# Kernel tuning notes

Hardware: AMD Instinct MI355X
Metric: run time of the kernel (lower is better)

Reference implementation:

```python
import jax, jax.numpy as jnp
import numpy as np

SOS = 1  # vocab.word2idx[SYM_SOS]


def _lstm_cell(x, h, c, Wih, Whh, b):
    # PyTorch LSTMCell gate order: i, f, g, o
    g = x @ Wih.T + h @ Whh.T + b
    i, f, gg, o = jnp.split(g, 4, axis=-1)
    c2 = jax.nn.sigmoid(f) * c + jax.nn.sigmoid(i) * jnp.tanh(gg)
    h2 = jax.nn.sigmoid(o) * jnp.tanh(c2)
    return h2, c2


def _attention(q, m, Wq, Wm, b, v):
    # additive attention: q [B,Dq], m [B,N,Dm] -> context [B,Dm]
    e = jnp.tanh((q @ Wq)[:, None, :] + m @ Wm + b)      # [B,N,H]
    score = jnp.einsum('bnh,h->bn', e, v)                # [B,N]
    a = jax.nn.softmax(score, axis=-1)
    return jnp.einsum('bn,bnd->bd', a, m)


def setup_inputs() -> dict:
    key = jax.random.key(0)
    ks = iter(jax.random.split(key, 32))
    B, T, V = 128, 20, 20000
    DI, DW, H = 512, 512, 1024
    s = 0.02
    d = {}
    d['img_feats'] = jax.random.normal(next(ks), (B, 36, DI), jnp.float32)
    d['ppl_feats'] = jax.random.normal(next(ks), (B, 100, DI), jnp.float32)
    d['answer_hint'] = jax.random.normal(next(ks), (B, DW), jnp.float32)
    d['question'] = jax.random.randint(next(ks), (B, T), 0, V)
    d['emb'] = jax.random.normal(next(ks), (V, DW), jnp.float32) * s
    d['pool_Wq'] = jax.random.normal(next(ks), (DW, DW), jnp.float32) * s
    d['pool_Wm'] = jax.random.normal(next(ks), (DI, DW), jnp.float32) * s
    d['pool_b'] = jnp.zeros((DW,), jnp.float32)
    d['pool_v'] = jax.random.normal(next(ks), (DW,), jnp.float32) * s
    d['img_Wq'] = jax.random.normal(next(ks), (H, H), jnp.float32) * s
    d['img_Wm'] = jax.random.normal(next(ks), (DI, H), jnp.float32) * s
    d['img_b'] = jnp.zeros((H,), jnp.float32)
    d['img_v'] = jax.random.normal(next(ks), (H,), jnp.float32) * s
    d['ppl_Wq'] = jax.random.normal(next(ks), (H, H), jnp.float32) * s
    d['ppl_Wm'] = jax.random.normal(next(ks), (DI, H), jnp.float32) * s
    d['ppl_b'] = jnp.zeros((H,), jnp.float32)
    d['ppl_v'] = jax.random.normal(next(ks), (H,), jnp.float32) * s
    d['vis_Wih'] = jax.random.normal(next(ks), (4 * H, DI + DW), jnp.float32) * s
    d['vis_Whh'] = jax.random.normal(next(ks), (4 * H, H), jnp.float32) * s
    d['vis_b'] = jnp.zeros((4 * H,), jnp.float32)
    d['lang_Wih'] = jax.random.normal(next(ks), (4 * H, H + DI), jnp.float32) * s
    d['lang_Whh'] = jax.random.normal(next(ks), (4 * H, H), jnp.float32) * s
    d['lang_b'] = jnp.zeros((4 * H,), jnp.float32)
    d['proj_W'] = jax.random.normal(next(ks), (H, V), jnp.float32) * s
    d['proj_b'] = jnp.zeros((V,), jnp.float32)
    return d


def reference(img_feats, ppl_feats, answer_hint, question, emb,
              pool_Wq, pool_Wm, pool_b, pool_v,
              img_Wq, img_Wm, img_b, img_v,
              ppl_Wq, ppl_Wm, ppl_b, ppl_v,
              vis_Wih, vis_Whh, vis_b,
              lang_Wih, lang_Whh, lang_b,
              proj_W, proj_b):
    B, T = question.shape
    H = vis_Whh.shape[1]
    # pooled image feature from answer hint (computed once)
    img_pool = _attention(answer_hint, img_feats, pool_Wq, pool_Wm, pool_b, pool_v)
    # teacher forcing inputs: SOS then question[:, :-1]
    tokens_in = jnp.concatenate(
        [jnp.full((B, 1), SOS, question.dtype), question[:, :-1]], axis=1)

    def step(carry, tok):
        h_vis, c_vis, h_lang, c_lang = carry
        dec_emb = jax.nn.relu(emb[tok])                          # [B,DW]
        x_vis = jnp.concatenate([img_pool, dec_emb], axis=-1)
        h_vis, c_vis = _lstm_cell(x_vis, h_vis, c_vis, vis_Wih, vis_Whh, vis_b)
        image_attn = _attention(h_vis, img_feats, img_Wq, img_Wm, img_b, img_v)
        ppl_attn = _attention(h_vis, ppl_feats, ppl_Wq, ppl_Wm, ppl_b, ppl_v)
        x_lang = jnp.concatenate([image_attn + ppl_attn, h_vis], axis=-1)
        h_lang, c_lang = _lstm_cell(x_lang, h_lang, c_lang, lang_Wih, lang_Whh, lang_b)
        logp = jax.nn.log_softmax(h_lang @ proj_W + proj_b, axis=-1)
        return (h_vis, c_vis, h_lang, c_lang), (logp, jnp.argmax(logp, axis=-1))

    z = jnp.zeros((B, H), img_feats.dtype)
    _, (logps, toks) = jax.lax.scan(step, (z, z, z, z), tokens_in.T)
    return jnp.transpose(logps, (1, 0, 2)), toks.T


if __name__ == '__main__':
    out = reference(**setup_inputs())
    print(out[0].shape, out[1].shape)
```

## Files before the change

### kernel.cpp

```cpp
#include <hip/hip_runtime.h>
#include <cstddef>
#include <cstdint>

using u16 = unsigned short;
typedef float    f32x4 __attribute__((ext_vector_type(4)));
typedef _Float16 f16x8 __attribute__((ext_vector_type(8)));
typedef u16      us8   __attribute__((ext_vector_type(8)));

constexpr int B  = 128;
constexpr int T  = 20;
constexpr int V  = 20000;
constexpr int DW = 512;
constexpr int H  = 1024;
constexpr int G4 = 4096;
constexpr int NI = 36;
constexpr int NP = 100;
constexpr int SOS = 1;

__device__ __forceinline__ float sigf(float x) { return 1.0f / (1.0f + expf(-x)); }
__device__ __forceinline__ u16 f16bits(_Float16 h) { u16 u; __builtin_memcpy(&u, &h, 2); return u; }
__device__ __forceinline__ float h2f(u16 u) { _Float16 h; __builtin_memcpy(&h, &u, 2); return (float)h; }

template<bool WSIDE>
__device__ __forceinline__ void split1(float x, u16& b0, u16& b1, u16& b2) {
    _Float16 h  = (_Float16)x;
    float    hf = (float)h;
    _Float16 lo = (_Float16)((x - hf) * 64.0f);
    _Float16 hs = (_Float16)(hf * (1.0f / 64.0f));
    b0 = f16bits(h);
    if constexpr (WSIDE) { b1 = f16bits(hs); b2 = f16bits(lo); }
    else                 { b1 = f16bits(lo); b2 = f16bits(hs); }
}

template<int BM, int BN, bool HAS_ADD, bool HAS_BIAS, int NSW = 0, bool OUTF16 = false>
__global__ __launch_bounds__(256)
void gemm3(const u16* __restrict__ A, const u16* __restrict__ Bt,
           const float* __restrict__ Add, const float* __restrict__ bias,
           void* __restrict__ Cv, int N, int K3)
{
    __shared__ __align__(16) u16 As[BM * 64];
    __shared__ __align__(16) u16 Bs[BN * 64];
    constexpr int FR = BM / 32, FC = BN / 32, PA = BM / 32, PB = BN / 32;
    const int tid  = threadIdx.x;
    int bx = blockIdx.x, by = blockIdx.y;
    if constexpr (NSW > 0) {
        const int nt = (int)gridDim.x, mt = (int)gridDim.y;
        const int lin = by * nt + bx;
        const int sc0 = (lin / (NSW * mt)) * NSW;
        const int w   = (NSW < nt - sc0) ? NSW : (nt - sc0);
        const int r   = lin - sc0 * mt;
        bx = sc0 + r % w;
        by = r / w;
    }
    const int bm   = by * BM, bn = bx * BN;
    const int lane = tid & 63, wid = tid >> 6;
    const int wm   = (wid >> 1) * (BM / 2), wn = (wid & 1) * (BN / 2);
    const int srow = tid >> 3;
    const int scol = (tid & 7) * 8;

    f32x4 acc[FR][FC] = {};
    us8 ra[PA], rb[PB];

    auto ldg = [&](int k0) {
#pragma unroll
        for (int p = 0; p < PA; ++p)
            ra[p] = *(const us8*)(A + (size_t)(bm + p * 32 + srow) * K3 + k0 + scol);
#pragma unroll
        for (int p = 0; p < PB; ++p) {
            int n = bn + p * 32 + srow; if (n > N - 1) n = N - 1;
            rb[p] = *(const us8*)(Bt + (size_t)n * K3 + k0 + scol);
        }
    };
    ldg(0);

    for (int k0 = 0; k0 < K3; k0 += 64) {
        __syncthreads();
#pragma unroll
        for (int p = 0; p < PA; ++p) {
            const int row = p * 32 + srow;
            *(us8*)((char*)As + row * 128 + ((scol * 2) ^ ((row & 7) << 4))) = ra[p];
        }
#pragma unroll
        for (int p = 0; p < PB; ++p) {
            const int row = p * 32 + srow;
            *(us8*)((char*)Bs + row * 128 + ((scol * 2) ^ ((row & 7) << 4))) = rb[p];
        }
        __syncthreads();
        if (k0 + 64 < K3) ldg(k0 + 64);
#pragma unroll
        for (int ks = 0; ks < 2; ++ks) {
            f16x8 af[FR], bf[FC];
#pragma unroll
            for (int m = 0; m < FR; ++m) {
                const int row = wm + m * 16 + (lane & 15);
                const int cb  = (ks * 64 + ((lane >> 4) << 4)) ^ ((row & 7) << 4);
                af[m] = *(const f16x8*)((const char*)As + row * 128 + cb);
            }
#pragma unroll
            for (int n = 0; n < FC; ++n) {
                const int row = wn + n * 16 + (lane & 15);
                const int cb  = (ks * 64 + ((lane >> 4) << 4)) ^ ((row & 7) << 4);
                bf[n] = *(const f16x8*)((const char*)Bs + row * 128 + cb);
            }
#pragma unroll
            for (int m = 0; m < FR; ++m)
#pragma unroll
                for (int n = 0; n < FC; ++n)
                    acc[m][n] = __builtin_amdgcn_mfma_f32_16x16x32_f16(af[m], bf[n], acc[m][n], 0, 0, 0);
        }
    }
#pragma unroll
    for (int m = 0; m < FR; ++m) {
        const int r0 = bm + wm + m * 16 + ((lane >> 4) << 2);
#pragma unroll
        for (int n = 0; n < FC; ++n) {
            const int c = bn + wn + n * 16 + (lane & 15);
            if (c < N) {
#pragma unroll
                for (int j = 0; j < 4; ++j) {
                    float v = acc[m][n][j];
                    if constexpr (HAS_ADD)  v += Add[(size_t)(r0 + j) * N + c];
                    if constexpr (HAS_BIAS) v += bias[c];
                    if constexpr (OUTF16)
                        ((u16*)Cv)[(size_t)(r0 + j) * N + c] = f16bits((_Float16)v);
                    else
                        ((float*)Cv)[(size_t)(r0 + j) * N + c] = v;
                }
            }
        }
    }
}

template<int EPI, int BN, int BK>
__device__ __forceinline__ void gemm_core(
    u16* __restrict__ As, u16* __restrict__ Bs,
    const u16* __restrict__ A, const u16* __restrict__ Bt,
    const float* __restrict__ Add, const float* __restrict__ bias,
    float* __restrict__ CS, u16* __restrict__ o1, u16* __restrict__ o2,
    int N, int K3, int t, int bx, int by)
{
    constexpr int NA8  = BK / 32;
    constexpr int TPRB = 256 / BN;
    constexpr int NB8  = (BK / TPRB) / 8;
    constexpr int NFC  = BN / 16;
    const int tid  = threadIdx.x;
    const int bn   = bx * BN, bm = by * 64;
    const int lane = tid & 63, wv = tid >> 6;
    const int rowA = tid >> 2;
    const int scA  = (tid & 3) * (BK / 4);
    const int rowB = tid / TPRB;
    const int scB  = (tid % TPRB) * (BK / TPRB);
    const int swzA = (rowA & 7) << 4;
    const int swzB = (rowB & 7) << 4;
    const u16* Ap = A  + (size_t)(bm + rowA) * K3 + scA;
    const u16* Bp = Bt + (size_t)(bn + rowB) * K3 + scB;
    char* Awp = (char*)As + rowA * (BK * 2);
    char* Bwp = (char*)Bs + rowB * (BK * 2);
    const int arow = wv * 16 + (lane & 15);
    const char* Arp = (const char*)As + arow * (BK * 2);
    const int aswz = (arow & 7) << 4;
    const int jl   = lane & 15;

    f32x4 acc[NFC] = {};
    us8 ra[NA8], rb[NB8];
#pragma unroll
    for (int i = 0; i < NA8; ++i) ra[i] = *(const us8*)(Ap + 8 * i);
#pragma unroll
    for (int i = 0; i < NB8; ++i) rb[i] = *(const us8*)(Bp + 8 * i);

    for (int k0 = 0; k0 < K3; k0 += BK) {
        __syncthreads();
#pragma unroll
        for (int i = 0; i < NA8; ++i)
            *(us8*)(Awp + ((scA * 2 + 16 * i) ^ swzA)) = ra[i];
#pragma unroll
        for (int i = 0; i < NB8; ++i)
            *(us8*)(Bwp + ((scB * 2 + 16 * i) ^ swzB)) = rb[i];
        __syncthreads();
        if (k0 + BK < K3) {
#pragma unroll
            for (int i = 0; i < NA8; ++i) ra[i] = *(const us8*)(Ap + k0 + BK + 8 * i);
#pragma unroll
            for (int i = 0; i < NB8; ++i) rb[i] = *(const us8*)(Bp + k0 + BK + 8 * i);
        }
#pragma unroll
        for (int ks = 0; ks < BK / 32; ++ks) {
            const int cb = ks * 64 + ((lane >> 4) << 4);
            const f16x8 af = *(const f16x8*)(Arp + (cb ^ aswz));
#pragma unroll
            for (int g = 0; g < NFC; ++g) {
                const int brow = g * 16 + jl;
                const f16x8 bf = *(const f16x8*)((const char*)Bs + brow * (BK * 2) + (cb ^ ((brow & 7) << 4)));
                acc[g] = __builtin_amdgcn_mfma_f32_16x16x32_f16(af, bf, acc[g], 0, 0, 0);
            }
        }
    }
    const int rb0 = bm + wv * 16 + ((lane >> 4) << 2);
    if constexpr (EPI == 0) {
#pragma unroll
        for (int g = 0; g < NFC; ++g) {
            const int c = bn + g * 16 + jl;
#pragma unroll
            for (int jj = 0; jj < 4; ++jj)
                CS[(size_t)(rb0 + jj) * N + c] = acc[g][jj];
        }
    } else {
        const int j = bx * 16 + jl;
#pragma unroll
        for (int jj = 0; jj < 4; ++jj) {
            const int b = rb0 + jj;
            float gi = acc[0][jj], gf = acc[1][jj], gg = acc[2][jj], go = acc[3][jj];
            if constexpr (EPI == 1) {
                const float* ap = Add + (size_t)b * 4096 + bn + jl;
                gi += ap[0]; gf += ap[16]; gg += ap[32]; go += ap[48];
            } else {
                const float* bp = bias + bn + jl;
                gi += bp[0]; gf += bp[16]; gg += bp[32]; go += bp[48];
            }
            const float c = sigf(gf) * CS[b * 1024 + j] + sigf(gi) * tanhf(gg);
            const float h = sigf(go) * tanhf(c);
            CS[b * 1024 + j] = c;
            u16 b0, b1, b2; split1<false>(h, b0, b1, b2);
            if constexpr (EPI == 1) {
                u16* a = o1 + (size_t)b * 3072 + j;
                a[0] = b0; a[1024] = b1; a[2048] = b2;
                u16* x = o2 + (size_t)b * 7680 + 512 + j;
                x[0] = b0; x[2560] = b1; x[5120] = b2;
            } else {
                u16* x = o1 + (size_t)b * 7680 + 1536 + j;
                x[0] = b0; x[2560] = b1; x[5120] = b2;
                u16* hh = o2 + ((size_t)b * T + t) * 3072 + j;
                hh[0] = b0; hh[1024] = b1; hh[2048] = b2;
            }
        }
    }
}

__global__ __launch_bounds__(256)
void gemm_q(const u16* __restrict__ A, const u16* __restrict__ Bt,
            float* __restrict__ CS, int N, int K3)
{
    __shared__ __align__(16) u16 As[64 * 384];
    __shared__ __align__(16) u16 Bs[32 * 384];
    gemm_core<0, 32, 384>(As, Bs, A, Bt, nullptr, nullptr, CS, nullptr, nullptr,
                          N, K3, 0, blockIdx.x, blockIdx.y);
}

__global__ __launch_bounds__(256)
void step_combo(const u16* __restrict__ lang_A, const u16* __restrict__ langW3,
                const float* __restrict__ lang_bi, float* __restrict__ c_lang,
                u16* __restrict__ lang_o1, u16* __restrict__ h3_all,
                const u16* __restrict__ vis_A, const u16* __restrict__ visWhh3,
                const float* __restrict__ g_pre_t, float* __restrict__ c_vis,
                u16* __restrict__ vis_o1, u16* __restrict__ vis_o2, int t)
{
    __shared__ __align__(16) u16 As[64 * 384];
    __shared__ __align__(16) u16 Bs[64 * 384];
    if (blockIdx.z == 0) {
        if (t >= 1)
            gemm_core<2, 64, 384>(As, Bs, lang_A, langW3, nullptr, lang_bi,
                                  c_lang, lang_o1, h3_all, G4, 7680, t - 1,
                                  blockIdx.x, blockIdx.y);
    } else {
        if (t < T)
            gemm_core<1, 64, 384>(As, Bs, vis_A, visWhh3, g_pre_t, nullptr,
                                  c_vis, vis_o1, vis_o2, G4, 3072, t,
                                  blockIdx.x, blockIdx.y);
    }
}

template<bool WSIDE>
__global__ __launch_bounds__(256)
void split3_rows(const float* __restrict__ src, int ld, int K8,
                 u16* __restrict__ out, int Kt, int coloff)
{
    const int idx = blockIdx.x * 256 + threadIdx.x;
    const int r = idx / K8, kk = (idx - r * K8) * 8;
    const float* s = src + (size_t)r * ld + kk;
    const float4 x0 = *(const float4*)s, x1 = *(const float4*)(s + 4);
    float xs[8] = {x0.x, x0.y, x0.z, x0.w, x1.x, x1.y, x1.z, x1.w};
    us8 h, m, l;
#pragma unroll
    for (int j = 0; j < 8; ++j) { u16 a, b, c; split1<WSIDE>(xs[j], a, b, c); h[j]=a; m[j]=b; l[j]=c; }
    u16* o = out + (size_t)r * (3 * Kt) + coloff + kk;
    *(us8*)o = h; *(us8*)(o + Kt) = m; *(us8*)(o + 2 * Kt) = l;
}

__global__ __launch_bounds__(256)
void split3_lstm(const float* __restrict__ src, int ld, int K8,
                 u16* __restrict__ out, int Kt, int coloff)
{
    const int idx = blockIdx.x * 256 + threadIdx.x;
    const int r = idx / K8, kk = (idx - r * K8) * 8;
    const int g = r >> 10, j = r & 1023;
    const int orow = ((j >> 4) << 6) + (g << 4) + (j & 15);
    const float* s = src + (size_t)r * ld + kk;
    const float4 x0 = *(const float4*)s, x1 = *(const float4*)(s + 4);
    float xs[8] = {x0.x, x0.y, x0.z, x0.w, x1.x, x1.y, x1.z, x1.w};
    us8 h, m, l;
#pragma unroll
    for (int jj = 0; jj < 8; ++jj) { u16 a, b, c; split1<true>(xs[jj], a, b, c); h[jj]=a; m[jj]=b; l[jj]=c; }
    u16* o = out + (size_t)orow * (3 * Kt) + coloff + kk;
    *(us8*)o = h; *(us8*)(o + Kt) = m; *(us8*)(o + 2 * Kt) = l;
}

__global__ __launch_bounds__(256)
void permute_bias_lstm(const float* __restrict__ b, float* __restrict__ out)
{
    const int c = blockIdx.x * 256 + threadIdx.x;
    const int jg = c >> 6, g = (c >> 4) & 3, jlo = c & 15;
    out[c] = b[g * 1024 + jg * 16 + jlo];
}

__global__ __launch_bounds__(256)
void transpose_split3_w(const float* __restrict__ W, int N, int K,
                        u16* __restrict__ out)
{
    const int n0 = blockIdx.x * 64, k0 = blockIdx.y * 64;
    const int tid = threadIdx.x;
    __shared__ float ts[64][65];
    for (int i = 0; i < 16; ++i) {
        const int idx = i * 256 + tid;
        const int kl = idx >> 6, nl = idx & 63;
        float v = 0.f;
        if (n0 + nl < N) v = W[(size_t)(k0 + kl) * N + n0 + nl];
        ts[nl][kl] = v;
    }
    __syncthreads();
    for (int i = 0; i < 2; ++i) {
        const int idx = i * 256 + tid;
        const int nl = idx >> 3, kc = (idx & 7) * 8;
        if (n0 + nl < N) {
            us8 h, m, l;
#pragma unroll
            for (int j = 0; j < 8; ++j) {
                u16 a, b, c; split1<true>(ts[nl][kc + j], a, b, c);
                h[j] = a; m[j] = b; l[j] = c;
            }
            u16* o = out + (size_t)(n0 + nl) * (3 * K) + k0 + kc;
            *(us8*)o = h; *(us8*)(o + K) = m; *(us8*)(o + 2 * K) = l;
        }
    }
}

__global__ __launch_bounds__(256)
void embed_relu3(const int* __restrict__ question, const float* __restrict__ emb,
                 u16* __restrict__ demb3)
{
    const int idx = blockIdx.x * 256 + threadIdx.x;
    const int r = idx >> 6, kk = (idx & 63) * 8;
    const int t = r / B, b = r - t * B;
    const int tok = (t == 0) ? SOS : question[b * T + t - 1];
    const float* s = emb + (size_t)tok * DW + kk;
    const float4 x0 = *(const float4*)s, x1 = *(const float4*)(s + 4);
    float xs[8] = {x0.x, x0.y, x0.z, x0.w, x1.x, x1.y, x1.z, x1.w};
    us8 h, m, l;
#pragma unroll
    for (int j = 0; j < 8; ++j) {
        u16 a, b2, c; split1<false>(fmaxf(xs[j], 0.f), a, b2, c);
        h[j] = a; m[j] = b2; l[j] = c;
    }
    u16* o = demb3 + (size_t)r * 1536 + kk;
    *(us8*)o = h; *(us8*)(o + 512) = m; *(us8*)(o + 1024) = l;
}

__global__ __launch_bounds__(256)
void attn_score(const float* __restrict__ q, int qld,
                const float* __restrict__ mW, const float* __restrict__ v,
                float* __restrict__ score, int Nn, int Hd)
{
    const int n = blockIdx.x, b = blockIdx.y;
    const float* qp = q + (size_t)b * qld;
    const float* mp = mW + ((size_t)b * Nn + n) * Hd;
    float s = 0.f;
    for (int h = threadIdx.x; h < Hd; h += 256)
        s += tanhf(qp[h] + mp[h]) * v[h];
    __shared__ float red[4];
    const int lane = threadIdx.x & 63, wv = threadIdx.x >> 6;
    for (int o = 32; o; o >>= 1) s += __shfl_down(s, o, 64);
    if (lane == 0) red[wv] = s;
    __syncthreads();
    if (threadIdx.x == 0) score[(size_t)b * Nn + n] = red[0] + red[1] + red[2] + red[3];
}

__global__ __launch_bounds__(256)
void attn_ctx_pool(const float* __restrict__ score, const float* __restrict__ m,
                   u16* __restrict__ out3, int Nn)
{
    constexpr int D = 512;
    const int b = blockIdx.x;
    __shared__ float aw[128];
    __shared__ float red[8];
    const int tid = threadIdx.x, lane = tid & 63, wv = tid >> 6;
    float mx = -3.4e38f;
    for (int n = tid; n < Nn; n += 256) mx = fmaxf(mx, score[(size_t)b * Nn + n]);
    for (int o = 32; o; o >>= 1) mx = fmaxf(mx, __shfl_down(mx, o, 64));
    if (lane == 0) red[wv] = mx;
    __syncthreads();
    mx = fmaxf(fmaxf(red[0], red[1]), fmaxf(red[2], red[3]));
    float se = 0.f;
    for (int n = tid; n < Nn; n += 256) {
        float e = expf(score[(size_t)b * Nn + n] - mx);
        aw[n] = e; se += e;
    }
    for (int o = 32; o; o >>= 1) se += __shfl_down(se, o, 64);
    if (lane == 0) red[4 + wv] = se;
    __syncthreads();
    const float inv = 1.0f / (red[4] + red[5] + red[6] + red[7]);
    for (int d = tid; d < D; d += 256) {
        float s = 0.f;
        for (int n = 0; n < Nn; ++n) s += aw[n] * m[((size_t)b * Nn + n) * D + d];
        s *= inv;
        u16 b0, b1, b2; split1<false>(s, b0, b1, b2);
        u16* o = out3 + (size_t)b * 1536 + d;
        o[0] = b0; o[512] = b1; o[1024] = b2;
    }
}

__global__ __launch_bounds__(512)
void attn_fused(const float* __restrict__ qbuf,
                const u16* __restrict__ img_mW, const u16* __restrict__ ppl_mW,
                const float* __restrict__ img_v, const float* __restrict__ ppl_v,
                const float* __restrict__ img_feats, const float* __restrict__ ppl_feats,
                u16* __restrict__ x3)
{
    const int b = blockIdx.x;
    const int tid = threadIdx.x, lane = tid & 63, wv = tid >> 6;
    __shared__ float qs[2048];
    __shared__ float vs[2048];
    __shared__ float aw[136];
    __shared__ float awn[136];

    for (int i = tid; i < 2048; i += 512) {
        qs[i] = qbuf[(size_t)b * 2048 + i];
        vs[i] = (i < 1024) ? img_v[i] : ppl_v[i - 1024];
    }
    __syncthreads();

    for (int n = wv; n < NI; n += 8) {
        const u16* mp = img_mW + ((size_t)b * NI + n) * 1024;
        float s = 0.f;
#pragma unroll
        for (int u = 0; u < 2; ++u) {
            const int h = (lane + 64 * u) * 8;
            const us8 m8 = *(const us8*)(mp + h);
#pragma unroll
            for (int j = 0; j < 8; ++j)
                s += tanhf(qs[h + j] + h2f(m8[j])) * vs[h + j];
        }
        for (int o = 1; o < 64; o <<= 1) s += __shfl_xor(s, o, 64);
        if (lane == 0) aw[n] = s;
    }
    for (int n = wv; n < NP; n += 8) {
        const u16* mp = ppl_mW + ((size_t)b * NP + n) * 1024;
        float s = 0.f;
#pragma unroll
        for (int u = 0; u < 2; ++u) {
            const int h = (lane + 64 * u) * 8;
            const us8 m8 = *(const us8*)(mp + h);
#pragma unroll
            for (int j = 0; j < 8; ++j)
                s += tanhf(qs[1024 + h + j] + h2f(m8[j])) * vs[1024 + h + j];
        }
        for (int o = 1; o < 64; o <<= 1) s += __shfl_xor(s, o, 64);
        if (lane == 0) aw[36 + n] = s;
    }
    __syncthreads();

    if (wv == 0) {
        const float x = (lane < NI) ? aw[lane] : -3.4e38f;
        float mx = x;
        for (int o = 1; o < 64; o <<= 1) mx = fmaxf(mx, __shfl_xor(mx, o, 64));
        const float e = (lane < NI) ? expf(x - mx) : 0.f;
        float ss = e;
        for (int o = 1; o < 64; o <<= 1) ss += __shfl_xor(ss, o, 64);
        if (lane < NI) awn[lane] = e / ss;
    } else if (wv == 1) {
        const float x0 = aw[36 + lane];
        const float x1 = (lane < NP - 64) ? aw[100 + lane] : -3.4e38f;
        float mx = fmaxf(x0, x1);
        for (int o = 1; o < 64; o <<= 1) mx = fmaxf(mx, __shfl_xor(mx, o, 64));
        const float e0 = expf(x0 - mx);
        const float e1 = (lane < NP - 64) ? expf(x1 - mx) : 0.f;
        float ss = e0 + e1;
        for (int o = 1; o < 64; o <<= 1) ss += __shfl_xor(ss, o, 64);
        awn[36 + lane] = e0 / ss;
        if (lane < NP - 64) awn[100 + lane] = e1 / ss;
    }
    __syncthreads();

    {
        const int d = tid;
        float s = 0.f;
        const float* ip = img_feats + (size_t)b * NI * 512 + d;
#pragma unroll 4
        for (int n = 0; n < NI; ++n) s += awn[n] * ip[n * 512];
        const float* pp = ppl_feats + (size_t)b * NP * 512 + d;
#pragma unroll 4
        for (int n = 0; n < NP; ++n) s += awn[36 + n] * pp[n * 512];
        u16 b0, b1, b2; split1<false>(s, b0, b1, b2);
        u16* o = x3 + (size_t)b * 7680 + d;
        o[0] = b0; o[2560] = b1; o[5120] = b2;
    }
}

__global__ __launch_bounds__(256)
void add_bcast(float* __restrict__ g_pre, const float* __restrict__ g_const)
{
    const int idx = blockIdx.x * 256 + threadIdx.x;
    const int bg = idx % (B * G4 / 4);
    float4 a = ((float4*)g_pre)[idx];
    const float4 c = ((const float4*)g_const)[bg];
    a.x += c.x; a.y += c.y; a.z += c.z; a.w += c.w;
    ((float4*)g_pre)[idx] = a;
}

__global__ __launch_bounds__(256)
void zero_f(float* __restrict__ p) { p[blockIdx.x * 256 + threadIdx.x] = 0.f; }

__global__ __launch_bounds__(256)
void zero_u32(unsigned int* __restrict__ p) { p[blockIdx.x * 256 + threadIdx.x] = 0u; }

__global__ __launch_bounds__(256)
void logsm_argmax(float* __restrict__ out)
{
    const int r = blockIdx.x;
    float* row = out + (size_t)r * V;
    const int tid = threadIdx.x, lane = tid & 63, wv = tid >> 6;
    float m = -3.4e38f, s = 0.f; int mi = 0;
    for (int i4 = tid; i4 < V / 4; i4 += 256) {
        const float4 x4 = ((const float4*)row)[i4];
        const float xs[4] = {x4.x, x4.y, x4.z, x4.w};
#pragma unroll
        for (int j = 0; j < 4; ++j) {
            const float x = xs[j];
            if (x > m) { s = s * expf(m - x) + 1.f; m = x; mi = i4 * 4 + j; }
            else       s += expf(x - m);
        }
    }
    for (int o = 1; o < 64; o <<= 1) {
        const float m2 = __shfl_xor(m, o, 64);
        const float s2 = __shfl_xor(s, o, 64);
        const int  mi2 = __shfl_xor(mi, o, 64);
        if (m2 > m || (m2 == m && mi2 < mi)) { s = s2 + s * expf(m - m2); m = m2; mi = mi2; }
        else s += s2 * expf(m2 - m);
    }
    __shared__ float sm[4], ssm[4]; __shared__ int smi[4];
    __shared__ float lse_sh; __shared__ int mi_sh;
    if (lane == 0) { sm[wv] = m; ssm[wv] = s; smi[wv] = mi; }
    __syncthreads();
    if (tid == 0) {
        float M = sm[0], S = ssm[0]; int MI = smi[0];
        for (int w = 1; w < 4; ++w) {
            if (sm[w] > M || (sm[w] == M && smi[w] < MI)) { S = ssm[w] + S * expf(M - sm[w]); M = sm[w]; MI = smi[w]; }
            else S += ssm[w] * expf(sm[w] - M);
        }
        lse_sh = M + logf(S); mi_sh = MI;
    }
    __syncthreads();
    const float lse = lse_sh;
    for (int i4 = tid; i4 < V / 4; i4 += 256) {
        float4 x4 = ((const float4*)row)[i4];
        x4.x -= lse; x4.y -= lse; x4.z -= lse; x4.w -= lse;
        ((float4*)row)[i4] = x4;
    }
    if (tid == 0) out[(size_t)B * T * V + r] = (float)mi_sh;
}

extern "C" void kernel_launch(void* const* d_in, const int* in_sizes, int n_in,
                              void* d_out, int out_size, void* d_ws, size_t ws_size,
                              hipStream_t stream)
{
    (void)in_sizes; (void)n_in; (void)out_size; (void)ws_size;

    const float* img_feats   = (const float*)d_in[0];
    const float* ppl_feats   = (const float*)d_in[1];
    const float* answer_hint = (const float*)d_in[2];
    const int*   question    = (const int*)d_in[3];
    const float* emb         = (const float*)d_in[4];
    const float* pool_Wq     = (const float*)d_in[5];
    const float* pool_Wm     = (const float*)d_in[6];
    const float* pool_b      = (const float*)d_in[7];
    const float* pool_v      = (const float*)d_in[8];
    const float* img_Wq      = (const float*)d_in[9];
    const float* img_Wm      = (const float*)d_in[10];
    const float* img_b       = (const float*)d_in[11];
    const float* img_v       = (const float*)d_in[12];
    const float* ppl_Wq      = (const float*)d_in[13];
    const float* ppl_Wm      = (const float*)d_in[14];
    const float* ppl_b       = (const float*)d_in[15];
    const float* ppl_v       = (const float*)d_in[16];
    const float* vis_Wih     = (const float*)d_in[17];
    const float* vis_Whh     = (const float*)d_in[18];
    const float* vis_b       = (const float*)d_in[19];
    const float* lang_Wih    = (const float*)d_in[20];
    const float* lang_Whh    = (const float*)d_in[21];
    const float* lang_b      = (const float*)d_in[22];
    const float* proj_W      = (const float*)d_in[23];
    const float* proj_b      = (const float*)d_in[24];

    float* out = (float*)d_out;
    float* ws  = (float*)d_ws;

    size_t off = 0;
    auto alloc = [&](size_t nf) { size_t r = off; off += (nf + 63) & ~(size_t)63; return r; };
    const size_t regionX = off;
    float* g_pre   = ws + alloc((size_t)T * B * G4);
    float* pool_mW = ws + alloc((size_t)B * NI * DW);
    u16*   demb3   = (u16*)(ws + alloc((size_t)T * B * 1536 / 2));
    u16*   hint3   = (u16*)(ws + alloc((size_t)B * 1536 / 2));
    u16*   poolWq3t= (u16*)(ws + alloc((size_t)512 * 1536 / 2));
    u16*   poolWm3t= (u16*)(ws + alloc((size_t)512 * 1536 / 2));
    u16*   visdemb3= (u16*)(ws + alloc((size_t)G4 * 1536 / 2));
    u16*   vispool3= (u16*)(ws + alloc((size_t)G4 * 1536 / 2));
    u16* img_mW    = (u16*)(ws + alloc((size_t)B * NI * H / 2));
    u16* ppl_mW    = (u16*)(ws + alloc((size_t)B * NP * H / 2));
    u16* img3      = (u16*)(ws + alloc((size_t)B * NI * 1536 / 2));
    u16* ppl3      = (u16*)(ws + alloc((size_t)B * NP * 1536 / 2));
    u16* imgpool3  = (u16*)(ws + alloc((size_t)B * 1536 / 2));
    u16* visWhh3   = (u16*)(ws + alloc((size_t)G4 * 3072 / 2));
    u16* langW3    = (u16*)(ws + alloc((size_t)G4 * 7680 / 2));
    u16* wq3t      = (u16*)(ws + alloc((size_t)2048 * 3072 / 2));
    u16* imgWm3t   = (u16*)(ws + alloc((size_t)1024 * 1536 / 2));
    u16* pplWm3t   = (u16*)(ws + alloc((size_t)1024 * 1536 / 2));
    float* c_vis   = ws + alloc((size_t)B * H);
    float* c_lang  = ws + alloc((size_t)B * H);
    u16* a3        = (u16*)(ws + alloc((size_t)2 * B * 3072 / 2));
    u16* x3        = (u16*)(ws + alloc((size_t)2 * B * 7680 / 2));
    u16* h3_all    = (u16*)(ws + alloc((size_t)B * T * 3072 / 2));
    float* qbuf    = ws + alloc((size_t)B * 2048);
    float* g_const = ws + alloc((size_t)B * G4);
    float* vis_bi  = ws + alloc((size_t)G4);
    float* lang_bi = ws + alloc((size_t)G4);
    float* pool_qW = ws + alloc((size_t)B * DW);
    float* pool_sc = ws + alloc((size_t)B * NI);
    u16* projW3t   = (u16*)(ws + regionX);

    const dim3 blk(256);

    zero_f<<<dim3((2 * B * H) / 256), blk, 0, stream>>>(c_vis);
    zero_u32<<<dim3((2 * B * 3072 + 2 * B * 7680) / 2 / 256), blk, 0, stream>>>((unsigned int*)a3);

    embed_relu3<<<dim3(T * B * 64 / 256), blk, 0, stream>>>(question, emb, demb3);
    permute_bias_lstm<<<dim3(16), blk, 0, stream>>>(vis_b, vis_bi);
    permute_bias_lstm<<<dim3(16), blk, 0, stream>>>(lang_b, lang_bi);
    split3_lstm<<<dim3(G4 * 64 / 256), blk, 0, stream>>>(vis_Wih + 512, 1024, 64, visdemb3, 512, 0);
    split3_lstm<<<dim3(G4 * 64 / 256), blk, 0, stream>>>(vis_Wih, 1024, 64, vispool3, 512, 0);
    split3_lstm<<<dim3(G4 * 128 / 256), blk, 0, stream>>>(vis_Whh, 1024, 128, visWhh3, 1024, 0);
    split3_lstm<<<dim3(G4 * 192 / 256), blk, 0, stream>>>(lang_Wih, 1536, 192, langW3, 2560, 0);
    split3_lstm<<<dim3(G4 * 128 / 256), blk, 0, stream>>>(lang_Whh, 1024, 128, langW3, 2560, 1536);
    split3_rows<false><<<dim3(B * NI * 64 / 256), blk, 0, stream>>>(img_feats, 512, 64, img3, 512, 0);
    split3_rows<false><<<dim3(B * NP * 64 / 256), blk, 0, stream>>>(ppl_feats, 512, 64, ppl3, 512, 0);
    split3_rows<false><<<dim3(B * 64 / 256), blk, 0, stream>>>(answer_hint, 512, 64, hint3, 512, 0);
    transpose_split3_w<<<dim3(8, 8), blk, 0, stream>>>(pool_Wq, 512, 512, poolWq3t);
    transpose_split3_w<<<dim3(8, 8), blk, 0, stream>>>(pool_Wm, 512, 512, poolWm3t);
    transpose_split3_w<<<dim3(16, 8), blk, 0, stream>>>(img_Wm, 1024, 512, imgWm3t);
    transpose_split3_w<<<dim3(16, 8), blk, 0, stream>>>(ppl_Wm, 1024, 512, pplWm3t);
    transpose_split3_w<<<dim3(16, 16), blk, 0, stream>>>(img_Wq, 1024, 1024, wq3t);
    transpose_split3_w<<<dim3(16, 16), blk, 0, stream>>>(ppl_Wq, 1024, 1024, wq3t + (size_t)1024 * 3072);

    gemm3<128, 128, false, true><<<dim3(32, 20), blk, 0, stream>>>(demb3, visdemb3, nullptr, vis_bi, g_pre, G4, 1536);
    gemm3<64, 64, false, false><<<dim3(8, 2), blk, 0, stream>>>(hint3, poolWq3t, nullptr, nullptr, pool_qW, 512, 1536);
    gemm3<128, 128, false, true><<<dim3(4, 36), blk, 0, stream>>>(img3, poolWm3t, nullptr, pool_b, pool_mW, 512, 1536);
    attn_score<<<dim3(NI, B), blk, 0, stream>>>(pool_qW, 512, pool_mW, pool_v, pool_sc, NI, 512);
    attn_ctx_pool<<<dim3(B), blk, 0, stream>>>(pool_sc, img_feats, imgpool3, NI);
    gemm3<64, 64, false, false><<<dim3(64, 2), blk, 0, stream>>>(imgpool3, vispool3, nullptr, nullptr, g_const, G4, 1536);
    add_bcast<<<dim3(T * B * G4 / 4 / 256), blk, 0, stream>>>(g_pre, g_const);
    gemm3<128, 128, false, true, 0, true><<<dim3(8, 36), blk, 0, stream>>>(img3, imgWm3t, nullptr, img_b, img_mW, H, 1536);
    gemm3<128, 128, false, true, 0, true><<<dim3(8, 100), blk, 0, stream>>>(ppl3, pplWm3t, nullptr, ppl_b, ppl_mW, H, 1536);

    for (int t = 0; t <= T; ++t) {
        u16* lang_A  = x3 + (size_t)((t + 1) & 1) * B * 7680;
        u16* lang_o1 = x3 + (size_t)(t & 1) * B * 7680;
        u16* vis_A   = a3 + (size_t)(t & 1) * B * 3072;
        u16* vis_o1  = a3 + (size_t)((t + 1) & 1) * B * 3072;
        u16* vis_o2  = x3 + (size_t)(t & 1) * B * 7680;
        const float* gp = g_pre + (size_t)(t < T ? t : 0) * B * G4;
        step_combo<<<dim3(64, 2, 2), blk, 0, stream>>>(
            lang_A, langW3, lang_bi, c_lang, lang_o1, h3_all,
            vis_A, visWhh3, gp, c_vis, vis_o1, vis_o2, t);
        if (t < T) {
            gemm_q<<<dim3(64, 2), blk, 0, stream>>>(vis_o1, wq3t, qbuf, 2048, 3072);
            attn_fused<<<dim3(B), dim3(512), 0, stream>>>(qbuf, img_mW, ppl_mW, img_v, ppl_v,
                                                          img_feats, ppl_feats, vis_o2);
        }
    }

    transpose_split3_w<<<dim3(313, 16), blk, 0, stream>>>(proj_W, V, 1024, projW3t);
    gemm3<128, 128, false, true, 20><<<dim3(157, 20), blk, 0, stream>>>(
        h3_all, projW3t, nullptr, proj_b, out, V, 3072);
    logsm_argmax<<<dim3(B * T), blk, 0, stream>>>(out);
}
```

Measured before the change: 3.658 ms.

## Fuse per-step decode kernels into one persistent kernel with grid barriers

The 20-step recurrent loop, which launched three kernels per step (LSTM GEMMs, query GEMM, attention), becomes a single persistent 256-block kernel. The stages are separated by software grid barriers built on atomics. Attention is split across two blocks per batch row, with scores exchanged through global memory. This removes about 60 kernel launches and their launch gaps, but adds barrier spin costs and assumes all 256 blocks are co-resident. The query GEMM now uses narrower tiles.

```diff
diff --git a/kernel.cpp b/kernel.cpp
--- a/kernel.cpp
+++ b/kernel.cpp
@@ -133,10 +133,10 @@
 
 template<int EPI, int BN, int BK>
 __device__ __forceinline__ void gemm_core(
-    u16* __restrict__ As, u16* __restrict__ Bs,
-    const u16* __restrict__ A, const u16* __restrict__ Bt,
-    const float* __restrict__ Add, const float* __restrict__ bias,
-    float* __restrict__ CS, u16* __restrict__ o1, u16* __restrict__ o2,
+    u16* As, u16* Bs,
+    const u16* A, const u16* Bt,
+    const float* Add, const float* bias,
+    float* CS, u16* o1, u16* o2,
     int N, int K3, int t, int bx, int by)
 {
     constexpr int NA8  = BK / 32;
@@ -236,36 +236,151 @@
     }
 }
 
-__global__ __launch_bounds__(256)
-void gemm_q(const u16* __restrict__ A, const u16* __restrict__ Bt,
-            float* __restrict__ CS, int N, int K3)
-{
-    __shared__ __align__(16) u16 As[64 * 384];
-    __shared__ __align__(16) u16 Bs[32 * 384];
-    gemm_core<0, 32, 384>(As, Bs, A, Bt, nullptr, nullptr, CS, nullptr, nullptr,
-                          N, K3, 0, blockIdx.x, blockIdx.y);
-}
-
-__global__ __launch_bounds__(256)
-void step_combo(const u16* __restrict__ lang_A, const u16* __restrict__ langW3,
-                const float* __restrict__ lang_bi, float* __restrict__ c_lang,
-                u16* __restrict__ lang_o1, u16* __restrict__ h3_all,
-                const u16* __restrict__ vis_A, const u16* __restrict__ visWhh3,
-                const float* __restrict__ g_pre_t, float* __restrict__ c_vis,
-                u16* __restrict__ vis_o1, u16* __restrict__ vis_o2, int t)
-{
-    __shared__ __align__(16) u16 As[64 * 384];
-    __shared__ __align__(16) u16 Bs[64 * 384];
-    if (blockIdx.z == 0) {
-        if (t >= 1)
-            gemm_core<2, 64, 384>(As, Bs, lang_A, langW3, nullptr, lang_bi,
-                                  c_lang, lang_o1, h3_all, G4, 7680, t - 1,
-                                  blockIdx.x, blockIdx.y);
-    } else {
-        if (t < T)
-            gemm_core<1, 64, 384>(As, Bs, vis_A, visWhh3, g_pre_t, nullptr,
-                                  c_vis, vis_o1, vis_o2, G4, 3072, t,
-                                  blockIdx.x, blockIdx.y);
+__device__ __forceinline__ void gridbar(unsigned* bar)
+{
+    __syncthreads();
+    if (threadIdx.x == 0) {
+        __threadfence();
+        unsigned* cnt = bar;
+        unsigned* gen = bar + 32;
+        unsigned g = __hip_atomic_load(gen, __ATOMIC_RELAXED, __HIP_MEMORY_SCOPE_AGENT);
+        if (__hip_atomic_fetch_add(cnt, 1u, __ATOMIC_ACQ_REL, __HIP_MEMORY_SCOPE_AGENT) == 255u) {
+            __hip_atomic_store(cnt, 0u, __ATOMIC_RELAXED, __HIP_MEMORY_SCOPE_AGENT);
+            __hip_atomic_store(gen, g + 1u, __ATOMIC_RELEASE, __HIP_MEMORY_SCOPE_AGENT);
+        } else {
+            while (__hip_atomic_load(gen, __ATOMIC_ACQUIRE, __HIP_MEMORY_SCOPE_AGENT) == g)
+                __builtin_amdgcn_s_sleep(2);
+        }
+        __threadfence();
+    }
+    __syncthreads();
+}
+
+__global__ __launch_bounds__(256, 1)
+void decode_mega(const u16* __restrict__ langW3, const float* __restrict__ lang_bi,
+                 float* c_lang,
+                 const u16* __restrict__ visWhh3, const float* __restrict__ g_pre,
+                 float* c_vis,
+                 const u16* __restrict__ wq3t,
+                 const u16* __restrict__ img_mW, const u16* __restrict__ ppl_mW,
+                 const float* __restrict__ img_v, const float* __restrict__ ppl_v,
+                 const float* __restrict__ img_feats, const float* __restrict__ ppl_feats,
+                 u16* a3, u16* x3, u16* h3_all,
+                 float* qbuf, float* scoreg, unsigned* bar)
+{
+    __shared__ __align__(16) u16 smem[2 * 64 * 384];
+    u16* As = smem;
+    u16* Bs = smem + 64 * 384;
+    float* smf = (float*)smem;
+    const int blk = blockIdx.x;
+    const int tid = threadIdx.x, lane = tid & 63, wv = tid >> 6;
+
+    for (int t = 0; t <= T; ++t) {
+        u16* lang_A = x3 + (size_t)((t + 1) & 1) * B * 7680;
+        u16* x3_cur = x3 + (size_t)(t & 1) * B * 7680;
+        u16* vis_A  = a3 + (size_t)(t & 1) * B * 3072;
+        u16* a3_new = a3 + (size_t)((t + 1) & 1) * B * 3072;
+
+        if (blk < 128) {
+            if (t >= 1)
+                gemm_core<2, 64, 384>(As, Bs, lang_A, langW3, nullptr, lang_bi,
+                                      c_lang, x3_cur, h3_all, G4, 7680, t - 1,
+                                      blk >> 1, blk & 1);
+        } else {
+            if (t < T)
+                gemm_core<1, 64, 384>(As, Bs, vis_A, visWhh3,
+                                      g_pre + (size_t)t * B * G4, nullptr,
+                                      c_vis, a3_new, x3_cur, G4, 3072, t,
+                                      (blk - 128) >> 1, (blk - 128) & 1);
+        }
+        if (t == T) break;
+        gridbar(bar);
+
+        gemm_core<0, 16, 384>(As, Bs, a3_new, wq3t, nullptr, nullptr,
+                              qbuf, nullptr, nullptr, 2048, 3072, t,
+                              blk & 127, blk >> 7);
+        gridbar(bar);
+
+        {
+            const int b = blk >> 1, h = blk & 1;
+            float* qs  = smf;
+            float* vsm = smf + 2048;
+            for (int i = tid; i < 2048; i += 256) {
+                qs[i]  = qbuf[(size_t)b * 2048 + i];
+                vsm[i] = (i < 1024) ? img_v[i] : ppl_v[i - 1024];
+            }
+            __syncthreads();
+            for (int n = h * 18 + wv; n < h * 18 + 18; n += 4) {
+                const u16* mp = img_mW + ((size_t)b * NI + n) * 1024;
+                float s = 0.f;
+#pragma unroll
+                for (int u = 0; u < 2; ++u) {
+                    const int hh = (lane + 64 * u) * 8;
+                    const us8 m8 = *(const us8*)(mp + hh);
+#pragma unroll
+                    for (int j = 0; j < 8; ++j)
+                        s += tanhf(qs[hh + j] + h2f(m8[j])) * vsm[hh + j];
+                }
+                for (int o = 1; o < 64; o <<= 1) s += __shfl_xor(s, o, 64);
+                if (lane == 0) scoreg[b * 136 + n] = s;
+            }
+            for (int n = h * 50 + wv; n < h * 50 + 50; n += 4) {
+                const u16* mp = ppl_mW + ((size_t)b * NP + n) * 1024;
+                float s = 0.f;
+#pragma unroll
+                for (int u = 0; u < 2; ++u) {
+                    const int hh = (lane + 64 * u) * 8;
+                    const us8 m8 = *(const us8*)(mp + hh);
+#pragma unroll
+                    for (int j = 0; j < 8; ++j)
+                        s += tanhf(qs[1024 + hh + j] + h2f(m8[j])) * vsm[1024 + hh + j];
+                }
+                for (int o = 1; o < 64; o <<= 1) s += __shfl_xor(s, o, 64);
+                if (lane == 0) scoreg[b * 136 + 36 + n] = s;
+            }
+        }
+        gridbar(bar);
+
+        {
+            const int b = blk >> 1, h = blk & 1;
+            float* aw  = smf;
+            float* awn = smf + 192;
+            for (int i = tid; i < 136; i += 256) aw[i] = scoreg[b * 136 + i];
+            __syncthreads();
+            if (wv == 0) {
+                const float x = (lane < NI) ? aw[lane] : -3.4e38f;
+                float mx = x;
+                for (int o = 1; o < 64; o <<= 1) mx = fmaxf(mx, __shfl_xor(mx, o, 64));
+                const float e = (lane < NI) ? expf(x - mx) : 0.f;
+                float ss = e;
+                for (int o = 1; o < 64; o <<= 1) ss += __shfl_xor(ss, o, 64);
+                if (lane < NI) awn[lane] = e / ss;
+            } else if (wv == 1) {
+                const float x0 = aw[36 + lane];
+                const float x1 = (lane < NP - 64) ? aw[100 + lane] : -3.4e38f;
+                float mx = fmaxf(x0, x1);
+                for (int o = 1; o < 64; o <<= 1) mx = fmaxf(mx, __shfl_xor(mx, o, 64));
+                const float e0 = expf(x0 - mx);
+                const float e1 = (lane < NP - 64) ? expf(x1 - mx) : 0.f;
+                float ss = e0 + e1;
+                for (int o = 1; o < 64; o <<= 1) ss += __shfl_xor(ss, o, 64);
+                awn[36 + lane] = e0 / ss;
+                if (lane < NP - 64) awn[100 + lane] = e1 / ss;
+            }
+            __syncthreads();
+            const int d = h * 256 + tid;
+            float s = 0.f;
+            const float* ip = img_feats + (size_t)b * NI * 512 + d;
+#pragma unroll 4
+            for (int n = 0; n < NI; ++n) s += awn[n] * ip[n * 512];
+            const float* pp = ppl_feats + (size_t)b * NP * 512 + d;
+#pragma unroll 4
+            for (int n = 0; n < NP; ++n) s += awn[36 + n] * pp[n * 512];
+            u16 b0, b1, b2; split1<false>(s, b0, b1, b2);
+            u16* o = x3_cur + (size_t)b * 7680 + d;
+            o[0] = b0; o[2560] = b1; o[5120] = b2;
+        }
+        gridbar(bar);
     }
 }
 
@@ -417,93 +532,6 @@
     }
 }
 
-__global__ __launch_bounds__(512)
-void attn_fused(const float* __restrict__ qbuf,
-                const u16* __restrict__ img_mW, const u16* __restrict__ ppl_mW,
-                const float* __restrict__ img_v, const float* __restrict__ ppl_v,
-                const float* __restrict__ img_feats, const float* __restrict__ ppl_feats,
-                u16* __restrict__ x3)
-{
-    const int b = blockIdx.x;
-    const int tid = threadIdx.x, lane = tid & 63, wv = tid >> 6;
-    __shared__ float qs[2048];
-    __shared__ float vs[2048];
-    __shared__ float aw[136];
-    __shared__ float awn[136];
-
-    for (int i = tid; i < 2048; i += 512) {
-        qs[i] = qbuf[(size_t)b * 2048 + i];
-        vs[i] = (i < 1024) ? img_v[i] : ppl_v[i - 1024];
-    }
-    __syncthreads();
-
-    for (int n = wv; n < NI; n += 8) {
-        const u16* mp = img_mW + ((size_t)b * NI + n) * 1024;
-        float s = 0.f;
-#pragma unroll
-        for (int u = 0; u < 2; ++u) {
-            const int h = (lane + 64 * u) * 8;
-            const us8 m8 = *(const us8*)(mp + h);
-#pragma unroll
-            for (int j = 0; j < 8; ++j)
-                s += tanhf(qs[h + j] + h2f(m8[j])) * vs[h + j];
-        }
-        for (int o = 1; o < 64; o <<= 1) s += __shfl_xor(s, o, 64);
-        if (lane == 0) aw[n] = s;
-    }
-    for (int n = wv; n < NP; n += 8) {
-        const u16* mp = ppl_mW + ((size_t)b * NP + n) * 1024;
-        float s = 0.f;
-#pragma unroll
-        for (int u = 0; u < 2; ++u) {
-            const int h = (lane + 64 * u) * 8;
-            const us8 m8 = *(const us8*)(mp + h);
-#pragma unroll
-            for (int j = 0; j < 8; ++j)
-                s += tanhf(qs[1024 + h + j] + h2f(m8[j])) * vs[1024 + h + j];
-        }
-        for (int o = 1; o < 64; o <<= 1) s += __shfl_xor(s, o, 64);
-        if (lane == 0) aw[36 + n] = s;
-    }
-    __syncthreads();
-
-    if (wv == 0) {
-        const float x = (lane < NI) ? aw[lane] : -3.4e38f;
-        float mx = x;
-        for (int o = 1; o < 64; o <<= 1) mx = fmaxf(mx, __shfl_xor(mx, o, 64));
-        const float e = (lane < NI) ? expf(x - mx) : 0.f;
-        float ss = e;
-        for (int o = 1; o < 64; o <<= 1) ss += __shfl_xor(ss, o, 64);
-        if (lane < NI) awn[lane] = e / ss;
-    } else if (wv == 1) {
-        const float x0 = aw[36 + lane];
-        const float x1 = (lane < NP - 64) ? aw[100 + lane] : -3.4e38f;
-        float mx = fmaxf(x0, x1);
-        for (int o = 1; o < 64; o <<= 1) mx = fmaxf(mx, __shfl_xor(mx, o, 64));
-        const float e0 = expf(x0 - mx);
-        const float e1 = (lane < NP - 64) ? expf(x1 - mx) : 0.f;
-        float ss = e0 + e1;
-        for (int o = 1; o < 64; o <<= 1) ss += __shfl_xor(ss, o, 64);
-        awn[36 + lane] = e0 / ss;
-        if (lane < NP - 64) awn[100 + lane] = e1 / ss;
-    }
-    __syncthreads();
-
-    {
-        const int d = tid;
-        float s = 0.f;
-        const float* ip = img_feats + (size_t)b * NI * 512 + d;
-#pragma unroll 4
-        for (int n = 0; n < NI; ++n) s += awn[n] * ip[n * 512];
-        const float* pp = ppl_feats + (size_t)b * NP * 512 + d;
-#pragma unroll 4
-        for (int n = 0; n < NP; ++n) s += awn[36 + n] * pp[n * 512];
-        u16 b0, b1, b2; split1<false>(s, b0, b1, b2);
-        u16* o = x3 + (size_t)b * 7680 + d;
-        o[0] = b0; o[2560] = b1; o[5120] = b2;
-    }
-}
-
 __global__ __launch_bounds__(256)
 void add_bcast(float* __restrict__ g_pre, const float* __restrict__ g_const)
 {
@@ -520,6 +548,8 @@
 
 __global__ __launch_bounds__(256)
 void zero_u32(unsigned int* __restrict__ p) { p[blockIdx.x * 256 + threadIdx.x] = 0u; }
+
+__global__ void zero_bar(unsigned* p) { p[threadIdx.x] = 0u; }
 
 __global__ __launch_bounds__(256)
 void logsm_argmax(float* __restrict__ out)
@@ -613,11 +643,11 @@
     u16*   poolWm3t= (u16*)(ws + alloc((size_t)512 * 1536 / 2));
     u16*   visdemb3= (u16*)(ws + alloc((size_t)G4 * 1536 / 2));
     u16*   vispool3= (u16*)(ws + alloc((size_t)G4 * 1536 / 2));
-    u16* img_mW    = (u16*)(ws + alloc((size_t)B * NI * H / 2));
-    u16* ppl_mW    = (u16*)(ws + alloc((size_t)B * NP * H / 2));
-    u16* img3      = (u16*)(ws + alloc((size_t)B * NI * 1536 / 2));
-    u16* ppl3      = (u16*)(ws + alloc((size_t)B * NP * 1536 / 2));
-    u16* imgpool3  = (u16*)(ws + alloc((size_t)B * 1536 / 2));
+    u16*   img_mW  = (u16*)(ws + alloc((size_t)B * NI * H / 2));
+    u16*   ppl_mW  = (u16*)(ws + alloc((size_t)B * NP * H / 2));
+    u16*   img3    = (u16*)(ws + alloc((size_t)B * NI * 1536 / 2));
+    u16*   ppl3    = (u16*)(ws + alloc((size_t)B * NP * 1536 / 2));
+    u16*   imgpool3= (u16*)(ws + alloc((size_t)B * 1536 / 2));
     u16* visWhh3   = (u16*)(ws + alloc((size_t)G4 * 3072 / 2));
     u16* langW3    = (u16*)(ws + alloc((size_t)G4 * 7680 / 2));
     u16* wq3t      = (u16*)(ws + alloc((size_t)2048 * 3072 / 2));
@@ -634,12 +664,15 @@
     float* lang_bi = ws + alloc((size_t)G4);
     float* pool_qW = ws + alloc((size_t)B * DW);
     float* pool_sc = ws + alloc((size_t)B * NI);
+    float* scoreg  = ws + alloc((size_t)B * 136);
+    unsigned* barp = (unsigned*)(ws + alloc(64));
     u16* projW3t   = (u16*)(ws + regionX);
 
     const dim3 blk(256);
 
     zero_f<<<dim3((2 * B * H) / 256), blk, 0, stream>>>(c_vis);
     zero_u32<<<dim3((2 * B * 3072 + 2 * B * 7680) / 2 / 256), blk, 0, stream>>>((unsigned int*)a3);
+    zero_bar<<<dim3(1), dim3(64), 0, stream>>>(barp);
 
     embed_relu3<<<dim3(T * B * 64 / 256), blk, 0, stream>>>(question, emb, demb3);
     permute_bias_lstm<<<dim3(16), blk, 0, stream>>>(vis_b, vis_bi);
@@ -669,22 +702,10 @@
     gemm3<128, 128, false, true, 0, true><<<dim3(8, 36), blk, 0, stream>>>(img3, imgWm3t, nullptr, img_b, img_mW, H, 1536);
     gemm3<128, 128, false, true, 0, true><<<dim3(8, 100), blk, 0, stream>>>(ppl3, pplWm3t, nullptr, ppl_b, ppl_mW, H, 1536);
 
-    for (int t = 0; t <= T; ++t) {
-        u16* lang_A  = x3 + (size_t)((t + 1) & 1) * B * 7680;
-        u16* lang_o1 = x3 + (size_t)(t & 1) * B * 7680;
-        u16* vis_A   = a3 + (size_t)(t & 1) * B * 3072;
-        u16* vis_o1  = a3 + (size_t)((t + 1) & 1) * B * 3072;
-        u16* vis_o2  = x3 + (size_t)(t & 1) * B * 7680;
-        const float* gp = g_pre + (size_t)(t < T ? t : 0) * B * G4;
-        step_combo<<<dim3(64, 2, 2), blk, 0, stream>>>(
-            lang_A, langW3, lang_bi, c_lang, lang_o1, h3_all,
-            vis_A, visWhh3, gp, c_vis, vis_o1, vis_o2, t);
-        if (t < T) {
-            gemm_q<<<dim3(64, 2), blk, 0, stream>>>(vis_o1, wq3t, qbuf, 2048, 3072);
-            attn_fused<<<dim3(B), dim3(512), 0, stream>>>(qbuf, img_mW, ppl_mW, img_v, ppl_v,
-                                                          img_feats, ppl_feats, vis_o2);
-        }
-    }
+    decode_mega<<<dim3(256), blk, 0, stream>>>(
+        langW3, lang_bi, c_lang, visWhh3, g_pre, c_vis, wq3t,
+        img_mW, ppl_mW, img_v, ppl_v, img_feats, ppl_feats,
+        a3, x3, h3_all, qbuf, scoreg, barp);
 
     transpose_split3_w<<<dim3(313, 16), blk, 0, stream>>>(proj_W, V, 1024, projW3t);
     gemm3<128, 128, false, true, 20><<<dim3(157, 20), blk, 0, stream>>>(
```

After: 7.524 ms. 2.06x slower.
